# Kernel tuning notes

Measured on AMD Instinct MI355X. Metric: run time of the kernel, lower is better.

The kernel has to match this reference:

```python
import jax, jax.numpy as jnp
import numpy as np


def setup_inputs() -> dict:
    key = jax.random.key(0)
    k1, k2 = jax.random.split(key)
    D = 512
    B, N = 32, 512
    panel_embeddings = jax.random.normal(k1, (B, N, D), dtype=jnp.float32)
    # nn.Bilinear(D, D, 1) weight: (1, D, D) -> squeeze to (D, D); bias: scalar
    bound = 1.0 / np.sqrt(D)
    W = jax.random.uniform(k2, (D, D), dtype=jnp.float32, minval=-bound, maxval=bound)
    b = jnp.float32(0.0)
    return {"panel_embeddings": panel_embeddings, "W": W, "b": b}


def reference(panel_embeddings, W, b):
    # score[b,i,j] = x_i^T W x_j + b, with diagonal forced to 0 (loop skips i==j)
    xw = jnp.einsum('bid,de->bie', panel_embeddings, W)          # (B, N, D)
    scores = jnp.einsum('bie,bje->bij', xw, panel_embeddings) + b  # (B, N, N)
    N = panel_embeddings.shape[1]
    mask = ~jnp.eye(N, dtype=bool)
    return jnp.where(mask, scores, jnp.zeros_like(scores))
```

## Files before the change

kernel.cpp:

```cpp
#include <hip/hip_runtime.h>
#include <stdint.h>

#define BATCH 32
#define NDIM 512
#define DDIM 512
#define XELEMS (BATCH * NDIM * DDIM)
#define WELEMS (DDIM * DDIM)
#define KITERS (DDIM / 64)

typedef _Float16 f16x8 __attribute__((ext_vector_type(8)));
typedef _Float16 f16x4v __attribute__((ext_vector_type(4)));
typedef float f32x4 __attribute__((ext_vector_type(4)));

__device__ __forceinline__ void gl_lds16(const _Float16* g, _Float16* l) {
    __builtin_amdgcn_global_load_lds(
        (const __attribute__((address_space(1))) unsigned int*)(g),
        (__attribute__((address_space(3))) unsigned int*)(l),
        16, 0, 0);
}

__global__ __launch_bounds__(256) void prep(const float4* __restrict__ X4,
                                            f16x4v* __restrict__ Xh4,
                                            const float* __restrict__ W,
                                            _Float16* __restrict__ Wt) {
    __shared__ float tile[32][33];
    int bid = blockIdx.x;
    if (bid < XELEMS / 4 / 256) {
        int i = bid * 256 + threadIdx.x;
        float4 v = X4[i];
        f16x4v o;
        o.x = (_Float16)v.x;
        o.y = (_Float16)v.y;
        o.z = (_Float16)v.z;
        o.w = (_Float16)v.w;
        Xh4[i] = o;
    } else {
        int t = bid - XELEMS / 4 / 256;
        int bx = t & 15;
        int by = t >> 4;
        int tx = threadIdx.x & 31;
        int ty = threadIdx.x >> 5;
        for (int r = ty; r < 32; r += 8)
            tile[r][tx] = W[(by * 32 + r) * DDIM + bx * 32 + tx];
        __syncthreads();
        for (int r = ty; r < 32; r += 8)
            Wt[(size_t)(bx * 32 + r) * DDIM + by * 32 + tx] = (_Float16)tile[tx][r];
    }
}

template <int EPI>
__global__ __launch_bounds__(256) void gemm_bt(const _Float16* __restrict__ A,
                                               const _Float16* __restrict__ Bt,
                                               _Float16* __restrict__ Yout,
                                               float* __restrict__ Sout,
                                               const float* __restrict__ bias_ptr) {
    __shared__ __align__(16) _Float16 As[128 * 64];
    __shared__ __align__(16) _Float16 Bs[64 * 64];

    const int tid  = threadIdx.x;
    const int lane = tid & 63;
    const int wv   = tid >> 6;

    int m0, n0, batch;
    if (EPI == 0) {
        int blk = blockIdx.x;
        n0 = (blk >> 7) * 64;
        m0 = (blk & 127) * 128;
        batch = 0;
    } else {
        int blk = blockIdx.x;
        batch = blk & 31;
        int t = blk >> 5;
        n0 = (t & 7) * 64;
        m0 = (t >> 3) * 128;
    }

    const _Float16* Ab = A;
    const _Float16* Bb = Bt;
    if (EPI == 1) {
        Ab = A  + (size_t)batch * (NDIM * DDIM);
        Bb = Bt + (size_t)batch * (NDIM * DDIM);
    }

    const int lr = lane >> 3;
    const int lc = lane & 7;
    const int lk = ((lc ^ lr) * 8);

    const _Float16* ga[4];
    const _Float16* gb[2];
#pragma unroll
    for (int t = 0; t < 4; ++t) {
        int chunk = wv * 4 + t;
        ga[t] = Ab + (size_t)(m0 + chunk * 8 + lr) * DDIM + lk;
    }
#pragma unroll
    for (int t = 0; t < 2; ++t) {
        int chunk = wv * 2 + t;
        gb[t] = Bb + (size_t)(n0 + chunk * 8 + lr) * DDIM + lk;
    }

    const int quad = lane >> 4;
    const int l16  = lane & 15;

    f32x4 acc[2][4];
#pragma unroll
    for (int i = 0; i < 2; ++i)
#pragma unroll
        for (int j = 0; j < 4; ++j)
            acc[i][j] = (f32x4){0.f, 0.f, 0.f, 0.f};

    for (int it = 0; it < KITERS; ++it) {
        const int k0 = it * 64;
#pragma unroll
        for (int t = 0; t < 4; ++t)
            gl_lds16(ga[t] + k0, &As[(wv * 4 + t) * 512]);
#pragma unroll
        for (int t = 0; t < 2; ++t)
            gl_lds16(gb[t] + k0, &Bs[(wv * 2 + t) * 512]);
        __syncthreads();

#pragma unroll
        for (int kkc = 0; kkc < 8; kkc += 4) {
            const int pa = (((kkc + quad) ^ (l16 & 7)) * 8);
            f16x8 a0 = *(const f16x8*)&As[(wv * 32 +      l16) * 64 + pa];
            f16x8 a1 = *(const f16x8*)&As[(wv * 32 + 16 + l16) * 64 + pa];
#pragma unroll
            for (int nt = 0; nt < 4; ++nt) {
                f16x8 b = *(const f16x8*)&Bs[(nt * 16 + l16) * 64 + pa];
                acc[0][nt] = __builtin_amdgcn_mfma_f32_16x16x32_f16(a0, b, acc[0][nt], 0, 0, 0);
                acc[1][nt] = __builtin_amdgcn_mfma_f32_16x16x32_f16(a1, b, acc[1][nt], 0, 0, 0);
            }
        }
        __syncthreads();
    }

    float bias = (EPI == 1) ? bias_ptr[0] : 0.f;
#pragma unroll
    for (int mt = 0; mt < 2; ++mt) {
#pragma unroll
        for (int nt = 0; nt < 4; ++nt) {
#pragma unroll
            for (int r = 0; r < 4; ++r) {
                int gi = m0 + wv * 32 + mt * 16 + quad * 4 + r;
                int gj = n0 + nt * 16 + l16;
                float v = acc[mt][nt][r];
                if (EPI == 0) {
                    Yout[(size_t)gi * DDIM + gj] = (_Float16)v;
                } else {
                    v += bias;
                    if (gi == gj) v = 0.f;
                    Sout[((size_t)batch * NDIM + gi) * NDIM + gj] = v;
                }
            }
        }
    }
}

extern "C" void kernel_launch(void* const* d_in, const int* in_sizes, int n_in,
                              void* d_out, int out_size, void* d_ws, size_t ws_size,
                              hipStream_t stream) {
    const float* X  = (const float*)d_in[0];
    const float* W  = (const float*)d_in[1];
    const float* bp = (const float*)d_in[2];
    float* out = (float*)d_out;

    _Float16* Xh = (_Float16*)d_ws;
    _Float16* Wt = Xh + XELEMS;
    _Float16* Y  = Wt + WELEMS;

    prep<<<XELEMS / 4 / 256 + 256, 256, 0, stream>>>((const float4*)X, (f16x4v*)Xh, W, Wt);

    gemm_bt<0><<<1024, 256, 0, stream>>>(Xh, Wt, Y, nullptr, nullptr);

    gemm_bt<1><<<1024, 256, 0, stream>>>(Y, Xh, nullptr, out, bp);

    (void)in_sizes; (void)n_in; (void)out_size; (void)ws_size;
}
```

Baseline: 112.8 us.

## Replace direct global-to-LDS loads with register-staged prefetch and padded LDS

Drops the global_load_lds path and instead loads the next K tile into registers while the current tile is consumed by MFMAs, then stores it to LDS. The XOR-swizzled layout becomes a row-padded layout (stride 72 halves) to avoid bank conflicts, and one barrier per iteration is removed. The aim is to overlap global memory latency with compute. The cost is extra VGPRs for the staging registers and extra LDS store instructions, which could reduce occupancy.

After: 116.4 us. 1.03x slower.

```diff
diff --git a/kernel.cpp b/kernel.cpp
--- a/kernel.cpp
+++ b/kernel.cpp
@@ -7,17 +7,11 @@
 #define XELEMS (BATCH * NDIM * DDIM)
 #define WELEMS (DDIM * DDIM)
 #define KITERS (DDIM / 64)
+#define LDA 72
 
 typedef _Float16 f16x8 __attribute__((ext_vector_type(8)));
 typedef _Float16 f16x4v __attribute__((ext_vector_type(4)));
 typedef float f32x4 __attribute__((ext_vector_type(4)));
-
-__device__ __forceinline__ void gl_lds16(const _Float16* g, _Float16* l) {
-    __builtin_amdgcn_global_load_lds(
-        (const __attribute__((address_space(1))) unsigned int*)(g),
-        (__attribute__((address_space(3))) unsigned int*)(l),
-        16, 0, 0);
-}
 
 __global__ __launch_bounds__(256) void prep(const float4* __restrict__ X4,
                                             f16x4v* __restrict__ Xh4,
@@ -54,8 +48,8 @@
                                                _Float16* __restrict__ Yout,
                                                float* __restrict__ Sout,
                                                const float* __restrict__ bias_ptr) {
-    __shared__ __align__(16) _Float16 As[128 * 64];
-    __shared__ __align__(16) _Float16 Bs[64 * 64];
+    __shared__ __align__(16) _Float16 As[128 * LDA];
+    __shared__ __align__(16) _Float16 Bs[64 * LDA];
 
     const int tid  = threadIdx.x;
     const int lane = tid & 63;
@@ -84,19 +78,21 @@
 
     const int lr = lane >> 3;
     const int lc = lane & 7;
-    const int lk = ((lc ^ lr) * 8);
 
     const _Float16* ga[4];
     const _Float16* gb[2];
+    int la[4], lb[2];
 #pragma unroll
     for (int t = 0; t < 4; ++t) {
-        int chunk = wv * 4 + t;
-        ga[t] = Ab + (size_t)(m0 + chunk * 8 + lr) * DDIM + lk;
+        int row = (wv * 4 + t) * 8 + lr;
+        ga[t] = Ab + (size_t)(m0 + row) * DDIM + lc * 8;
+        la[t] = row * LDA + lc * 8;
     }
 #pragma unroll
     for (int t = 0; t < 2; ++t) {
-        int chunk = wv * 2 + t;
-        gb[t] = Bb + (size_t)(n0 + chunk * 8 + lr) * DDIM + lk;
+        int row = (wv * 2 + t) * 8 + lr;
+        gb[t] = Bb + (size_t)(n0 + row) * DDIM + lc * 8;
+        lb[t] = row * LDA + lc * 8;
     }
 
     const int quad = lane >> 4;
@@ -109,29 +105,42 @@
         for (int j = 0; j < 4; ++j)
             acc[i][j] = (f32x4){0.f, 0.f, 0.f, 0.f};
 
+    f16x8 ra[4], rb[2];
+#pragma unroll
+    for (int t = 0; t < 4; ++t) ra[t] = *(const f16x8*)ga[t];
+#pragma unroll
+    for (int t = 0; t < 2; ++t) rb[t] = *(const f16x8*)gb[t];
+
+#pragma unroll
     for (int it = 0; it < KITERS; ++it) {
-        const int k0 = it * 64;
+        if (it > 0) __syncthreads();
+
 #pragma unroll
-        for (int t = 0; t < 4; ++t)
-            gl_lds16(ga[t] + k0, &As[(wv * 4 + t) * 512]);
+        for (int t = 0; t < 4; ++t) *(f16x8*)&As[la[t]] = ra[t];
 #pragma unroll
-        for (int t = 0; t < 2; ++t)
-            gl_lds16(gb[t] + k0, &Bs[(wv * 2 + t) * 512]);
+        for (int t = 0; t < 2; ++t) *(f16x8*)&Bs[lb[t]] = rb[t];
         __syncthreads();
+
+        if (it + 1 < KITERS) {
+            const int k1 = (it + 1) * 64;
+#pragma unroll
+            for (int t = 0; t < 4; ++t) ra[t] = *(const f16x8*)(ga[t] + k1);
+#pragma unroll
+            for (int t = 0; t < 2; ++t) rb[t] = *(const f16x8*)(gb[t] + k1);
+        }
 
 #pragma unroll
         for (int kkc = 0; kkc < 8; kkc += 4) {
-            const int pa = (((kkc + quad) ^ (l16 & 7)) * 8);
-            f16x8 a0 = *(const f16x8*)&As[(wv * 32 +      l16) * 64 + pa];
-            f16x8 a1 = *(const f16x8*)&As[(wv * 32 + 16 + l16) * 64 + pa];
+            const int pa = (kkc + quad) * 8;
+            f16x8 a0 = *(const f16x8*)&As[(wv * 32 +      l16) * LDA + pa];
+            f16x8 a1 = *(const f16x8*)&As[(wv * 32 + 16 + l16) * LDA + pa];
 #pragma unroll
             for (int nt = 0; nt < 4; ++nt) {
-                f16x8 b = *(const f16x8*)&Bs[(nt * 16 + l16) * 64 + pa];
+                f16x8 b = *(const f16x8*)&Bs[(nt * 16 + l16) * LDA + pa];
                 acc[0][nt] = __builtin_amdgcn_mfma_f32_16x16x32_f16(a0, b, acc[0][nt], 0, 0, 0);
                 acc[1][nt] = __builtin_amdgcn_mfma_f32_16x16x32_f16(a1, b, acc[1][nt], 0, 0, 0);
             }
         }
-        __syncthreads();
     }
 
     float bias = (EPI == 1) ? bias_ptr[0] : 0.f;
```
